# Kernel optimization log

Measured on AMD Instinct MI355X. Metric: run time of the kernel, lower is better.

The kernel has to match this reference:

```python
import jax, jax.numpy as jnp
import numpy as np

B, N = 4096, 8192
PULSE_LO = 40.0 / 60.0   # Hz
PULSE_HI = 250.0 / 60.0  # Hz


def setup_inputs() -> dict:
    key = jax.random.key(0)
    k1, k2 = jax.random.split(key)
    outputs = jax.random.normal(k1, (B, N), dtype=jnp.float32)
    # reference heart rates in Hz, uniform inside the pulse band
    targets = jax.random.uniform(k2, (B, 1), dtype=jnp.float32,
                                 minval=PULSE_LO, maxval=PULSE_HI)
    return {"outputs": outputs, "targets": targets, "Fs": 20}


def reference(outputs, targets, Fs):
    n = outputs.shape[-1]
    F = n // 2 + 1
    f = jnp.linspace(0.0, Fs / 2.0, F, dtype=jnp.float32)  # [F]

    min_idx = jnp.argmin(jnp.abs(f - PULSE_LO))
    max_idx = jnp.argmin(jnp.abs(f - PULSE_HI))

    # normalized rFFT power spectrum (torch.rfft(..., normalized=True) divides by sqrt(N))
    X = jnp.fft.rfft(outputs) * (1.0 / np.sqrt(n))          # [B, F] complex
    P1 = X.real ** 2 + X.imag ** 2                          # [B, F]

    # per-sample reference bin index
    r = jnp.argmin(jnp.abs(f[None, :] - targets.reshape(-1, 1)), axis=1)  # [B]
    rb = r[:, None]                                         # [B, 1]
    i = jnp.arange(F)[None, :]                              # [1, F]

    # signal mask u: 1 at ref and 1st harmonic, 0.5 at ref+-1 (applied after, as in torch)
    u = jnp.where((i == rb - 1) | (i == rb + 1), 0.5,
                  jnp.where((i == rb) | (i == 2 * rb), 1.0, 0.0))
    # noise mask w = 1 - u, zeroed outside pulse band and around 1st harmonic
    w = jnp.where((i < min_idx) | (i >= max_idx) |
                  (i == 2 * rb - 1) | (i == 2 * rb + 1),
                  0.0, 1.0 - u)

    signal_energy = jnp.sum(P1 * u, axis=1)                 # [B]
    noise_energy = jnp.sum(P1 * w, axis=1)                  # [B]
    losses = -10.0 * jnp.log(signal_energy / (noise_energy + 1.0)) / jnp.log(10.0)
    return jnp.mean(losses)
```

## Files before the change

### kernel.cpp

```cpp
#include <hip/hip_runtime.h>
#include <math.h>

#define TPB 256
#define ROWS 4

typedef float cplx __attribute__((ext_vector_type(2)));

typedef const __attribute__((address_space(1))) char gchar_t;
typedef __attribute__((address_space(3))) char lchar_t;

__device__ __forceinline__ cplx cmul(cplx a, cplx b) {
    return a.xx * b + cplx{-a.y, a.y} * b.yx;
}

__device__ __forceinline__ void dft4(cplx& a, cplx& b, cplx& c, cplx& d) {
    cplx t0 = a + c, t1 = a - c, t2 = b + d, t3 = b - d;
    a = t0 + t2;
    c = t0 - t2;
    cplx jt3 = cplx{t3.y, -t3.x};
    b = t1 + jt3;
    d = t1 - jt3;
}

#define T16(j) (4 * ((j) & 3) + ((j) >> 2))

__device__ __forceinline__ void dft16(cplx v[16]) {
#pragma unroll
    for (int j = 0; j < 4; ++j) dft4(v[j], v[4 + j], v[8 + j], v[12 + j]);
    const float C1 = 0.9238795325112867f, S1 = 0.3826834323650898f;
    const float R2 = 0.7071067811865476f;
    v[5]  = cmul(v[5],  cplx{ C1, -S1});
    v[9]  = cmul(v[9],  cplx{ R2, -R2});
    v[13] = cmul(v[13], cplx{ S1, -C1});
    v[6]  = cmul(v[6],  cplx{ R2, -R2});
    v[10] = cplx{v[10].y, -v[10].x};
    v[14] = cmul(v[14], cplx{-R2, -R2});
    v[7]  = cmul(v[7],  cplx{ S1, -C1});
    v[11] = cmul(v[11], cplx{-R2, -R2});
    v[15] = cmul(v[15], cplx{-C1,  S1});
#pragma unroll
    for (int b = 0; b < 4; ++b) dft4(v[4 * b], v[4 * b + 1], v[4 * b + 2], v[4 * b + 3]);
}

__device__ __forceinline__ void bar_lds() {
    asm volatile("s_waitcnt lgkmcnt(0)" ::: "memory");
    __builtin_amdgcn_s_barrier();
    asm volatile("" ::: "memory");
}

__device__ __forceinline__ void dma_row(const float* rowp, char* ldsbase,
                                        int wid, int lane) {
    const char* g = (const char*)rowp + wid * 8192 + lane * 16;
    char* l = ldsbase + wid * 8192;
#pragma unroll
    for (int j = 0; j < 8; ++j) {
        __builtin_amdgcn_global_load_lds((gchar_t*)(g + j * 1024),
                                         (lchar_t*)(l + j * 1024), 16, 0, 0);
    }
}

__global__ __launch_bounds__(TPB, 2) void snr_kernel(const float* __restrict__ x,
                                                     const float* __restrict__ targets,
                                                     float* __restrict__ out) {
    __shared__ __align__(16) cplx A[4096];
    __shared__ __align__(16) cplx B[4096];
    float* zf = (float*)B;

    const int t = threadIdx.x;
    const int tl = t & 15;
    const int rb = t ^ ((t >> 4) & 15);
    const int wbase = t << 4;
    const int row0 = blockIdx.x * ROWS;
    const int wid = t >> 6, lane = t & 63;

    cplx tw0[16], tw1[16], wkb[7];
    {
        float ang = -1.5339807878856412e-3f * (float)t;
        float sn, cs; __sincosf(ang, &sn, &cs);
        cplx w1 = cplx{cs, sn};
        cplx u2 = cmul(w1, w1), u3 = cmul(u2, w1);
        cplx v4 = cmul(u2, u2), v8 = cmul(v4, v4), v12 = cmul(v8, v4);
        cplx ua[4] = {cplx{1.f, 0.f}, w1, u2, u3};
        cplx vb[4] = {cplx{1.f, 0.f}, v4, v8, v12};
#pragma unroll
        for (int m = 0; m < 16; ++m) tw0[m] = cmul(vb[m >> 2], ua[m & 3]);
    }
    {
        float ang = -0.02454369260617026f * (float)(t >> 4);
        float sn, cs; __sincosf(ang, &sn, &cs);
        cplx w1 = cplx{cs, sn};
        cplx u2 = cmul(w1, w1), u3 = cmul(u2, w1);
        cplx v4 = cmul(u2, u2), v8 = cmul(v4, v4), v12 = cmul(v8, v4);
        cplx ua[4] = {cplx{1.f, 0.f}, w1, u2, u3};
        cplx vb[4] = {cplx{1.f, 0.f}, v4, v8, v12};
#pragma unroll
        for (int m = 0; m < 16; ++m) tw1[m] = cmul(vb[m >> 2], ua[m & 3]);
    }
    {
        float ang = -7.669903939428206e-4f * (float)t;
        float sn, cs; __sincosf(ang, &sn, &cs);
        cplx wku = cplx{cs, sn};
        const float WCc[7] = {1.f, 0.9807852804032304f, 0.9238795325112867f,
                              0.8314696123025452f, 0.7071067811865476f,
                              0.5555702330196022f, 0.3826834323650898f};
        const float WCs[7] = {0.f, -0.19509032201612825f, -0.3826834323650898f,
                              -0.5555702330196022f, -0.7071067811865476f,
                              -0.8314696123025452f, -0.9238795325112867f};
#pragma unroll
        for (int m = 1; m <= 6; ++m) wkb[m] = cmul(wku, cplx{WCc[m], WCs[m]});
    }

    dma_row(x + (size_t)row0 * 8192, (char*)A, wid, lane);
    __syncthreads();

    float lossSum = 0.f;

#pragma unroll 1
    for (int it = 0; it < ROWS; ++it) {
        cplx a[16];
#pragma unroll
        for (int l = 0; l < 16; ++l) a[l] = A[t + 256 * l];

        int r;
        {
            float tg = targets[row0 + it];
            const float df = 0.00244140625f;
            int c0 = (int)(tg * 409.6f) - 2;
            if (c0 < 0) c0 = 0;
            r = c0;
            float best = fabsf(df * (float)c0 - tg);
            for (int i = c0 + 1; i <= c0 + 4 && i <= 4096; ++i) {
                float dd = fabsf(df * (float)i - tg);
                if (dd < best) { best = dd; r = i; }
            }
        }

        dft16(a);
#pragma unroll
        for (int m = 1; m < 16; ++m) { int j = T16(m); a[j] = cmul(a[j], tw0[m]); }
#pragma unroll
        for (int j = 0; j < 16; ++j) B[wbase + (T16(j) ^ tl)] = a[j];
        bar_lds();

        if (it + 1 < ROWS) dma_row(x + (size_t)(row0 + it + 1) * 8192, (char*)A, wid, lane);

#pragma unroll
        for (int l = 0; l < 16; ++l) a[l] = B[rb + (l << 8)];
        bar_lds();
        dft16(a);
#pragma unroll
        for (int m = 1; m < 16; ++m) { int j = T16(m); a[j] = cmul(a[j], tw1[m]); }
        {
            const int base1 = (t >> 4) << 8;
#pragma unroll
            for (int m = 0; m < 16; ++m) B[base1 + (m << 4) + (tl ^ m)] = a[T16(m)];
        }
        bar_lds();

#pragma unroll
        for (int l = 0; l < 16; ++l) a[l] = B[rb + (l << 8)];
        bar_lds();
        dft16(a);

#pragma unroll
        for (int j = 0; j < 16; ++j) B[wbase + (T16(j) ^ tl)] = a[j];
        bar_lds();

        float band = 0.f;
        {
            const int pc = ((256 - t) & 255) << 4;
            const int pl = (16 - tl) & 15;
#pragma unroll
            for (int m = 1; m <= 6; ++m) {
                const int k = t + (m << 8);
                const int za = t ? (pc | ((15 - m) ^ pl)) : (16 - m);
                cplx Zk = a[T16(m)];
                cplx Zn = B[za];
                cplx Znc = cplx{Zn.x, -Zn.y};
                cplx s  = Zk + Znc;
                cplx dd = Zk - Znc;
                cplx tt = cmul(wkb[m], dd);
                cplx X  = s + cplx{tt.y, -tt.x};
                float P = (X.x * X.x + X.y * X.y) * (1.0f / 32768.0f);
                if ((unsigned)(k - 273) <= 1433u) band += P;
            }
        }

        float capP = 0.f;
        if (t < 6) {
            const int c = (t < 3) ? (r - 1 + t) : (2 * r - 4 + t);
            const int kk = (c <= 2048) ? c : (4096 - c);
            const int nb = (4096 - kk) & 4095;
            const int zka = ((kk & 255) << 4) | ((kk >> 8) ^ (kk & 15));
            const int zna = ((nb & 255) << 4) | ((nb >> 8) ^ (nb & 15));
            cplx Zk = B[zka], Zn = B[zna];
            float ang = -7.669903939428206e-4f * (float)kk;
            float sn, cs; __sincosf(ang, &sn, &cs);
            cplx wk = cplx{cs, sn};
            cplx Znc = cplx{Zn.x, -Zn.y};
            cplx s  = Zk + Znc;
            cplx dd = Zk - Znc;
            cplx tt = cmul(wk, dd);
            cplx X  = (c <= 2048) ? (s + cplx{tt.y, -tt.x})
                                  : (s + cplx{-tt.y, tt.x});
            capP = (X.x * X.x + X.y * X.y) * (1.0f / 32768.0f);
        }
        bar_lds();

        if (t < 6) zf[t] = capP;

#pragma unroll
        for (int off = 32; off > 0; off >>= 1) band += __shfl_down(band, off);
        if ((t & 63) == 0) zf[8 + (t >> 6)] = band;

        __syncthreads();

        if (t == 0) {
            float bb = zf[8] + zf[9] + zf[10] + zf[11];
            float S = zf[1] + zf[4] + 0.5f * (zf[0] + zf[2]);
            float noise = bb;
            const int r2 = 2 * r;
            if (r <= 1706)      noise -= zf[1];
            if (r - 1 >= 273)   noise -= 0.5f * zf[0];
            if (r + 1 <= 1706)  noise -= 0.5f * zf[2];
            if (r2 - 1 <= 1706) noise -= zf[3];
            if (r2 <= 1706)     noise -= zf[4];
            if (r2 + 1 <= 1706) noise -= zf[5];
            lossSum += -10.0f * log10f(S / (noise + 1.0f));
        }
    }

    if (t == 0) atomicAdd(out, lossSum * (1.0f / 4096.0f));
}

extern "C" void kernel_launch(void* const* d_in, const int* in_sizes, int n_in,
                              void* d_out, int out_size, void* d_ws, size_t ws_size,
                              hipStream_t stream) {
    const float* x = (const float*)d_in[0];
    const float* tg = (const float*)d_in[1];
    float* out = (float*)d_out;
    hipMemsetAsync(out, 0, sizeof(float), stream);
    snr_kernel<<<4096 / ROWS, TPB, 0, stream>>>(x, tg, out);
}
```

Measured before the change: 198.6 us.

## Pair conjugate FFT columns per wavefront to post-process real FFT via shuffles

Threads in the last radix-16 pass are remapped so that each thread's conjugate-partner column, 256-k, sits in the same wavefront at lane^32. The real-FFT split step then fetches Z[N-k] with cross-lane shuffles instead of writing the spectrum back to LDS and rereading it. This drops one LDS store/load round trip and two barriers per row. The six special capture bins are now picked out of the per-thread loop instead of being recomputed by six threads, and the per-thread twiddle setup is reworked. In exchange the mapping and edge cases (self-paired threads) are more intricate, and the loop now covers 13 bins per thread with extra predicate logic.

```diff
diff --git a/kernel.cpp b/kernel.cpp
--- a/kernel.cpp
+++ b/kernel.cpp
@@ -64,7 +64,7 @@
                                                      float* __restrict__ out) {
     __shared__ __align__(16) cplx A[4096];
     __shared__ __align__(16) cplx B[4096];
-    float* zf = (float*)B;
+    __shared__ float zfs[16];
 
     const int t = threadIdx.x;
     const int tl = t & 15;
@@ -73,7 +73,13 @@
     const int row0 = blockIdx.x * ROWS;
     const int wid = t >> 6, lane = t & 63;
 
-    cplx tw0[16], tw1[16], wkb[7];
+    int tp = (lane < 32) ? (32 * wid + 1 + lane) : (287 - 32 * wid - lane);
+    if (t == 255) tp = 0;
+    const bool self128 = (t == 223);
+    const bool self0   = (t == 255);
+    const int rb2 = tp ^ ((tp >> 4) & 15);
+
+    cplx tw0[16], tw1[16], wl;
     {
         float ang = -1.5339807878856412e-3f * (float)t;
         float sn, cs; __sincosf(ang, &sn, &cs);
@@ -97,18 +103,19 @@
         for (int m = 0; m < 16; ++m) tw1[m] = cmul(vb[m >> 2], ua[m & 3]);
     }
     {
-        float ang = -7.669903939428206e-4f * (float)t;
+        float ang = -7.669903939428206e-4f * (float)tp;
         float sn, cs; __sincosf(ang, &sn, &cs);
-        cplx wku = cplx{cs, sn};
-        const float WCc[7] = {1.f, 0.9807852804032304f, 0.9238795325112867f,
-                              0.8314696123025452f, 0.7071067811865476f,
-                              0.5555702330196022f, 0.3826834323650898f};
-        const float WCs[7] = {0.f, -0.19509032201612825f, -0.3826834323650898f,
-                              -0.5555702330196022f, -0.7071067811865476f,
-                              -0.8314696123025452f, -0.9238795325112867f};
-#pragma unroll
-        for (int m = 1; m <= 6; ++m) wkb[m] = cmul(wku, cplx{WCc[m], WCs[m]});
-    }
+        wl = cplx{cs, sn};
+    }
+
+    const float WMc[14] = {1.f, 0.9807852804f, 0.9238795325f, 0.8314696123f,
+                           0.7071067812f, 0.5555702330f, 0.3826834324f,
+                           0.1950903220f, 0.f, -0.1950903220f, -0.3826834324f,
+                           -0.5555702330f, -0.7071067812f, -0.8314696123f};
+    const float WMs[14] = {0.f, 0.1950903220f, 0.3826834324f, 0.5555702330f,
+                           0.7071067812f, 0.8314696123f, 0.9238795325f,
+                           0.9807852804f, 1.f, 0.9807852804f, 0.9238795325f,
+                           0.8314696123f, 0.7071067812f, 0.5555702330f};
 
     dma_row(x + (size_t)row0 * 8192, (char*)A, wid, lane);
     __syncthreads();
@@ -134,6 +141,13 @@
                 if (dd < best) { best = dd; r = i; }
             }
         }
+        int mA = -1, slotA = 0, mB = -1, slotB = 0;
+        {
+            int dA = (tp - (r - 1)) & 255;
+            if (dA < 3) { slotA = dA; mA = (r - 1 + dA) >> 8; }
+            int dB = (tp - (2 * r - 1)) & 255;
+            if (dB < 3) { slotB = 3 + dB; mB = (2 * r - 1 + dB) >> 8; }
+        }
 
         dft16(a);
 #pragma unroll
@@ -158,74 +172,56 @@
         bar_lds();
 
 #pragma unroll
-        for (int l = 0; l < 16; ++l) a[l] = B[rb + (l << 8)];
-        bar_lds();
+        for (int l = 0; l < 16; ++l) a[l] = B[rb2 + (l << 8)];
         dft16(a);
 
-#pragma unroll
-        for (int j = 0; j < 16; ++j) B[wbase + (T16(j) ^ tl)] = a[j];
-        bar_lds();
-
-        float band = 0.f;
-        {
-            const int pc = ((256 - t) & 255) << 4;
-            const int pl = (16 - tl) & 15;
-#pragma unroll
-            for (int m = 1; m <= 6; ++m) {
-                const int k = t + (m << 8);
-                const int za = t ? (pc | ((15 - m) ^ pl)) : (16 - m);
-                cplx Zk = a[T16(m)];
-                cplx Zn = B[za];
-                cplx Znc = cplx{Zn.x, -Zn.y};
-                cplx s  = Zk + Znc;
-                cplx dd = Zk - Znc;
-                cplx tt = cmul(wkb[m], dd);
-                cplx X  = s + cplx{tt.y, -tt.x};
-                float P = (X.x * X.x + X.y * X.y) * (1.0f / 32768.0f);
-                if ((unsigned)(k - 273) <= 1433u) band += P;
-            }
-        }
-
-        float capP = 0.f;
-        if (t < 6) {
-            const int c = (t < 3) ? (r - 1 + t) : (2 * r - 4 + t);
-            const int kk = (c <= 2048) ? c : (4096 - c);
-            const int nb = (4096 - kk) & 4095;
-            const int zka = ((kk & 255) << 4) | ((kk >> 8) ^ (kk & 15));
-            const int zna = ((nb & 255) << 4) | ((nb >> 8) ^ (nb & 15));
-            cplx Zk = B[zka], Zn = B[zna];
-            float ang = -7.669903939428206e-4f * (float)kk;
-            float sn, cs; __sincosf(ang, &sn, &cs);
-            cplx wk = cplx{cs, sn};
+        cplx sw[15];
+#pragma unroll
+        for (int j = 2; j <= 14; ++j) {
+            sw[j].x = __shfl_xor(a[T16(j)].x, 32);
+            sw[j].y = __shfl_xor(a[T16(j)].y, 32);
+        }
+
+        float band = 0.f, capA = 0.f, capB = 0.f;
+#pragma unroll
+        for (int m = 1; m <= 13; ++m) {
+            cplx Zk = a[T16(m)];
+            cplx Zn = sw[15 - m];
+            if (self128) Zn = a[T16(15 - m)];
+            if (self0)   Zn = a[T16((16 - m) & 15)];
             cplx Znc = cplx{Zn.x, -Zn.y};
             cplx s  = Zk + Znc;
             cplx dd = Zk - Znc;
+            cplx wk = cmul(wl, cplx{WMc[m], -WMs[m]});
             cplx tt = cmul(wk, dd);
-            cplx X  = (c <= 2048) ? (s + cplx{tt.y, -tt.x})
-                                  : (s + cplx{-tt.y, tt.x});
-            capP = (X.x * X.x + X.y * X.y) * (1.0f / 32768.0f);
-        }
-        bar_lds();
-
-        if (t < 6) zf[t] = capP;
+            cplx X  = s + cplx{tt.y, -tt.x};
+            float P = (X.x * X.x + X.y * X.y) * (1.0f / 32768.0f);
+            if (m >= 2 && m <= 5) band += P;
+            else if (m == 1) { if (tp >= 17)  band += P; }
+            else if (m == 6) { if (tp <= 170) band += P; }
+            if (m == mA) capA = P;
+            if (m == mB) capB = P;
+        }
+        if (mA >= 0) zfs[slotA] = capA;
+        if (mB >= 0) zfs[slotB] = capB;
 
 #pragma unroll
         for (int off = 32; off > 0; off >>= 1) band += __shfl_down(band, off);
-        if ((t & 63) == 0) zf[8 + (t >> 6)] = band;
+        if (lane == 0) zfs[8 + wid] = band;
 
         __syncthreads();
 
         if (t == 0) {
-            float bb = zf[8] + zf[9] + zf[10] + zf[11];
-            float S = zf[1] + zf[4] + 0.5f * (zf[0] + zf[2]);
+            float bb = zfs[8] + zfs[9] + zfs[10] + zfs[11];
+            float S = zfs[1] + zfs[4] + 0.5f * (zfs[0] + zfs[2]);
             float noise = bb;
             const int r2 = 2 * r;
-            if (r <= 1706)      noise -= zf[1];
-            if (r - 1 >= 273)   noise -= 0.5f * zf[0];
-            if (r + 1 <= 1706)  noise -= 0.5f * zf[2];
-            if (r2 - 1 <= 1706) noise -= zf[3];
-            if (r2 <= 1706)     noise -= zf[4];
-            if (r2 + 1 <= 1706) noise -= zf[5];
+            if (r <= 1706)      noise -= zfs[1];
+            if (r - 1 >= 273)   noise -= 0.5f * zfs[0];
+            if (r + 1 <= 1706)  noise -= 0.5f * zfs[2];
+            if (r2 - 1 <= 1706) noise -= zfs[3];
+            if (r2 <= 1706)     noise -= zfs[4];
+            if (r2 + 1 <= 1706) noise -= zfs[5];
             lossSum += -10.0f * log10f(S / (noise + 1.0f));
         }
     }
```

Measured after the change: 201.2 us. Within noise of the previous version (+1.3%).
